# Performance work log

Hardware: AMD Instinct MI355X
Metric: run time of the kernel (lower is better)

## Reference

```python
import jax, jax.numpy as jnp
import numpy as np

B, N, F_IN, F_OUT = 1024, 16, 1024, 4096  # n_nodes=16 and n_heads=1 are structurally fixed by the module


def setup_inputs() -> dict:
    key = jax.random.key(0)
    ks = jax.random.split(key, 7)
    s1 = 1.0 / np.sqrt(F_IN)
    s2 = 1.0 / np.sqrt(F_IN * 16)
    return {
        "x": jax.random.normal(ks[0], (B, N, F_IN), jnp.float32),
        "matrix": jax.random.uniform(ks[1], (B, N, N), jnp.float32),
        "W1": jax.random.uniform(ks[2], (F_IN, F_IN), jnp.float32, -s1, s1),
        "b1": jax.random.uniform(ks[3], (F_IN,), jnp.float32, -s1, s1),
        "W_mlp": jax.random.uniform(ks[4], (F_OUT, F_IN * 16), jnp.float32, -s2, s2),
        "b_mlp": jax.random.uniform(ks[5], (F_OUT,), jnp.float32, -s2, s2),
        "a_param": jnp.float32(5.0),
    }


def _l2norm(v):
    # matches F.normalize(p=2, dim=-1, eps=1e-12)
    n = jnp.maximum(jnp.linalg.norm(v, axis=-1, keepdims=True), 1e-12)
    return v / n


def _forward(x, matrix, W1, b1, W_mlp, b_mlp, a_param):
    Bc, n, f = x.shape  # n_heads = 1, n_hidden = f
    wg = x @ W1.T + b1                                    # [B,n,f]
    gs = _l2norm(x)                                       # g_reshaped (H=1)
    gt = _l2norm(wg)                                      # g_transposed
    e = jnp.einsum('bik,bjk->bij', gs, gt)[..., None]     # [B,n,n,1] cosine scores
    eye = jnp.eye(n, dtype=x.dtype)[None, :, :, None]
    e = e * (1.0 + eye * a_param)                         # boost diagonal
    a_scores = e                                          # pre-softmax scores (used below)
    esm = jax.nn.softmax(e, axis=1)                       # softmax over dim=1
    m = matrix[..., None]                                 # [B,n,n,1]
    # MPUGAT message passing
    from_i = jnp.einsum('bitp,btkp->bikp', esm, m)        # [B,n,n,1]
    diag = jnp.einsum('bkkp->bkp', m)                     # diagonal of matrix
    from_j = esm * diag[:, None, :, :]                    # '...jkp,...kkp->...jkp'
    e2 = jnp.einsum('bikp,bjkp->bijp', from_i, from_j)    # [B,n,n,1]
    e2 = 0.5 * (e2 + jnp.transpose(e2, (0, 2, 1, 3)))
    # attention readout with PRE-softmax scores a_scores
    g = x.reshape(Bc, n, 1, f)                            # [B,n,H=1,f]
    attn = jnp.tanh(jnp.einsum('bjhf,bjih->bihf', g, a_scores))  # [B,n,1,f]
    out = attn.reshape(Bc, -1) @ W_mlp.T + b_mlp          # [B,F_OUT]
    out = jnp.broadcast_to(out[:, None, :], (Bc, 16, out.shape[-1]))  # repeat(1,16,1)
    return out, e2, m


def reference(x, matrix, W1, b1, W_mlp, b_mlp, a_param):
    return _forward(x, matrix, W1, b1, W_mlp, b_mlp, a_param)
```

## Files before the change

### kernel.cpp

```cpp
#include <hip/hip_runtime.h>
#include <math.h>

typedef short short8 __attribute__((ext_vector_type(8)));
typedef float f32x4 __attribute__((ext_vector_type(4)));
typedef unsigned short us4 __attribute__((ext_vector_type(4)));
typedef unsigned int u32x4 __attribute__((ext_vector_type(4)));
typedef unsigned short u16;
typedef unsigned int u32;

#define GAS __attribute__((address_space(1)))
#define LAS __attribute__((address_space(3)))

static __device__ __forceinline__ u16 f2bf(float f) {
    union { float f; u32 u; } v; v.f = f;
    u32 r = v.u + 0x7FFFu + ((v.u >> 16) & 1u);
    return (u16)(r >> 16);
}

static __device__ __forceinline__ u32 pk2(float a, float b) {
    return (u32)f2bf(a) | ((u32)f2bf(b) << 16);
}

static __device__ __forceinline__ u32 cvtpk(float lo, float hi) {
    u32 r;
    asm("v_cvt_pk_bf16_f32 %0, %1, %2" : "=v"(r) : "v"(lo), "v"(hi));
    return r;
}

static __device__ __forceinline__ float bf2f(u16 h) {
    union { u32 u; float f; } v; v.u = ((u32)h) << 16;
    return v.f;
}

static __device__ __forceinline__ float ftanh(float v) {
    float t = __expf(-2.0f * fabsf(v));
    float r = (1.0f - t) / (1.0f + t);
    return copysignf(r, v);
}

static __device__ __forceinline__ void gll16(const void* g, void* l) {
    __builtin_amdgcn_global_load_lds((const GAS void*)g, (LAS void*)l, 16, 0, 0);
}

__global__ __launch_bounds__(256) void k_cvt_x(const float* __restrict__ x,
                                               u16* __restrict__ xb,
                                               float* __restrict__ xinv,
                                               const float* __restrict__ W1,
                                               u16* __restrict__ w1b) {
    const int bid = blockIdx.x, t = threadIdx.x;
    if (bid >= 16384) {
        const size_t i = (size_t)(bid - 16384) * 256 + t;
        const f32x4 v = *(const f32x4*)(W1 + 4 * i);
        u32* dst = (u32*)(w1b + 4 * i);
        dst[0] = pk2(v.x, v.y); dst[1] = pk2(v.z, v.w);
        return;
    }
    const int row = bid;
    const f32x4 v = *(const f32x4*)(x + (size_t)row * 1024 + 4 * t);
    u32* dst = (u32*)(xb + (size_t)row * 1024 + 4 * t);
    dst[0] = pk2(v.x, v.y); dst[1] = pk2(v.z, v.w);
    float s = v.x * v.x + v.y * v.y + v.z * v.z + v.w * v.w;
#pragma unroll
    for (int off = 1; off < 64; off <<= 1) s += __shfl_xor(s, off, 64);
    __shared__ float red[4];
    if ((t & 63) == 0) red[t >> 6] = s;
    __syncthreads();
    if (t == 0)
        xinv[row] = 1.0f / fmaxf(sqrtf(red[0] + red[1] + red[2] + red[3]), 1e-12f);
}

#define MFMA16(a, b, c) __builtin_amdgcn_mfma_f32_16x16x32_bf16(a, b, c, 0, 0, 0)
#define SBAR() __builtin_amdgcn_s_barrier()
#define SCHED0() __builtin_amdgcn_sched_barrier(0)
#define PHFENCE() do { SBAR(); SCHED0(); } while (0)
#define VMW4 asm volatile("s_waitcnt vmcnt(4)" ::: "memory")
#define VMW2 asm volatile("s_waitcnt vmcnt(2)" ::: "memory")
#define VMW0 asm volatile("s_waitcnt vmcnt(0)" ::: "memory")
#define VMW8L asm volatile("s_waitcnt vmcnt(8) lgkmcnt(0)" ::: "memory")
#define LGKML asm volatile("s_waitcnt lgkmcnt(0)" ::: "memory")
#define VMNOP do {} while (0)

#define DO_TILE(ISS, VMA, VMB, VMD)                                           \
  do {                                                                        \
    short8 Af[4][2], Bf0[2][2], Bf1[2][2];                                    \
    _Pragma("unroll") for (int m = 0; m < 4; ++m) {                           \
      Af[m][0] = *(const short8*)(la + rpA[m] + sw0);                         \
      Af[m][1] = *(const short8*)(la + rpA[m] + sw1);                         \
    }                                                                         \
    _Pragma("unroll") for (int n = 0; n < 2; ++n) {                           \
      Bf0[n][0] = *(const short8*)(lb + rpB[n] + sw0);                        \
      Bf0[n][1] = *(const short8*)(lb + rpB[n] + sw1);                        \
    }                                                                         \
    if (ISS) { gll16(AG + (saO00 + knx), danext + ldst);                      \
               gll16(AG + (saO01 + knx), danext + 4096 + ldst); }             \
    PHFENCE();                                                                \
    __builtin_amdgcn_s_setprio(1);                                            \
    _Pragma("unroll") for (int k = 0; k < 2; ++k)                             \
      _Pragma("unroll") for (int m = 0; m < 4; ++m)                           \
        _Pragma("unroll") for (int n = 0; n < 2; ++n)                         \
          acc[m][n] = MFMA16(Af[m][k], Bf0[n][k], acc[m][n]);                 \
    __builtin_amdgcn_s_setprio(0); SCHED0(); VMA; SBAR();                     \
    _Pragma("unroll") for (int n = 0; n < 2; ++n) {                           \
      Bf1[n][0] = *(const short8*)(lb + rpB[n + 2] + sw0);                    \
      Bf1[n][1] = *(const short8*)(lb + rpB[n + 2] + sw1);                    \
    }                                                                         \
    if (ISS) { gll16(BG + (sbO00 + knx), dbnext + ldst);                      \
               gll16(BG + (sbO01 + knx), dbnext + 4096 + ldst); }             \
    PHFENCE();                                                                \
    __builtin_amdgcn_s_setprio(1);                                            \
    _Pragma("unroll") for (int k = 0; k < 2; ++k)                             \
      _Pragma("unroll") for (int m = 0; m < 4; ++m)                           \
        _Pragma("unroll") for (int n = 0; n < 2; ++n)                         \
          acc[m][n + 2] = MFMA16(Af[m][k], Bf1[n][k], acc[m][n + 2]);         \
    __builtin_amdgcn_s_setprio(0); SCHED0(); VMB; SBAR();                     \
    _Pragma("unroll") for (int m = 0; m < 4; ++m) {                           \
      Af[m][0] = *(const short8*)(la + rpA[m + 4] + sw0);                     \
      Af[m][1] = *(const short8*)(la + rpA[m + 4] + sw1);                     \
    }                                                                         \
    if (ISS) { gll16(BG + (sbO10 + knx), dbnext + 8192 + ldst);               \
               gll16(BG + (sbO11 + knx), dbnext + 8192 + 4096 + ldst); }      \
    PHFENCE();                                                                \
    __builtin_amdgcn_s_setprio(1);                                            \
    _Pragma("unroll") for (int k = 0; k < 2; ++k)                             \
      _Pragma("unroll") for (int m = 0; m < 4; ++m)                           \
        _Pragma("unroll") for (int n = 0; n < 2; ++n)                         \
          acc[m + 4][n] = MFMA16(Af[m][k], Bf0[n][k], acc[m + 4][n]);         \
    __builtin_amdgcn_s_setprio(0); SCHED0();                                  \
    if (ISS) { gll16(AG + (saO10 + knx), danext + 8192 + ldst);               \
               gll16(AG + (saO11 + knx), danext + 8192 + 4096 + ldst); }      \
    __builtin_amdgcn_s_setprio(1);                                            \
    _Pragma("unroll") for (int k = 0; k < 2; ++k)                             \
      _Pragma("unroll") for (int m = 0; m < 4; ++m)                           \
        _Pragma("unroll") for (int n = 0; n < 2; ++n)                         \
          acc[m + 4][n + 2] = MFMA16(Af[m][k], Bf1[n][k], acc[m + 4][n + 2]); \
    __builtin_amdgcn_s_setprio(0); SCHED0(); VMD; SBAR();                     \
  } while (0)

#define GT2S(ISS, KNXA, KNXB, WAITX)                                          \
  do {                                                                        \
    short8 Af[4][2], Bf0[2][2], Bf1[2][2];                                    \
    _Pragma("unroll") for (int m = 0; m < 4; ++m) {                           \
      Af[m][0] = *(const short8*)(la + rpA[m] + sw0);                         \
      Af[m][1] = *(const short8*)(la + rpA[m] + sw1);                         \
    }                                                                         \
    _Pragma("unroll") for (int n = 0; n < 2; ++n) {                           \
      Bf0[n][0] = *(const short8*)(lb + rpB[n] + sw0);                        \
      Bf0[n][1] = *(const short8*)(lb + rpB[n] + sw1);                        \
    }                                                                         \
    if (ISS) { gll16(AG + (saO00 + (KNXA)), danext + ldst);                   \
               gll16(AG + (saO01 + (KNXA)), danext + 4096 + ldst); }          \
    PHFENCE();                                                                \
    __builtin_amdgcn_s_setprio(1);                                            \
    _Pragma("unroll") for (int k = 0; k < 2; ++k)                             \
      _Pragma("unroll") for (int m = 0; m < 4; ++m)                           \
        _Pragma("unroll") for (int n = 0; n < 2; ++n)                         \
          acc[m][n] = MFMA16(Af[m][k], Bf0[n][k], acc[m][n]);                 \
    __builtin_amdgcn_s_setprio(0); SCHED0(); SBAR();                          \
    _Pragma("unroll") for (int n = 0; n < 2; ++n) {                           \
      Bf1[n][0] = *(const short8*)(lb + rpB[n + 2] + sw0);                    \
      Bf1[n][1] = *(const short8*)(lb + rpB[n + 2] + sw1);                    \
    }                                                                         \
    if (ISS) { gll16(AG + (saO10 + (KNXA)), danext + 8192 + ldst);            \
               gll16(AG + (saO11 + (KNXA)), danext + 8192 + 4096 + ldst); }   \
    PHFENCE();                                                                \
    __builtin_amdgcn_s_setprio(1);                                            \
    _Pragma("unroll") for (int k = 0; k < 2; ++k)                             \
      _Pragma("unroll") for (int m = 0; m < 4; ++m)                           \
        _Pragma("unroll") for (int n = 0; n < 2; ++n)                         \
          acc[m][n + 2] = MFMA16(Af[m][k], Bf1[n][k], acc[m][n + 2]);         \
    __builtin_amdgcn_s_setprio(0); SCHED0(); SBAR();                          \
    _Pragma("unroll") for (int m = 0; m < 4; ++m) {                           \
      Af[m][0] = *(const short8*)(la + rpA[m + 4] + sw0);                     \
      Af[m][1] = *(const short8*)(la + rpA[m + 4] + sw1);                     \
    }                                                                         \
    PHFENCE();                                                                \
    __builtin_amdgcn_s_setprio(1);                                            \
    _Pragma("unroll") for (int k = 0; k < 2; ++k)                             \
      _Pragma("unroll") for (int m = 0; m < 4; ++m)                           \
        _Pragma("unroll") for (int n = 0; n < 2; ++n)                         \
          acc[m + 4][n] = MFMA16(Af[m][k], Bf0[n][k], acc[m + 4][n]);         \
    __builtin_amdgcn_s_setprio(0); SCHED0();                                  \
    if (ISS) {                                                                \
      _Pragma("unroll") for (int c = 0; c < 2; ++c) {                         \
        u32x4 wv;                                                             \
        wv.x = cvtpk(bn[2 * c].x, bn[2 * c].y);                               \
        wv.y = cvtpk(bn[2 * c].z, bn[2 * c].w);                               \
        wv.z = cvtpk(bn[2 * c + 1].x, bn[2 * c + 1].y);                       \
        wv.w = cvtpk(bn[2 * c + 1].z, bn[2 * c + 1].w);                       \
        *(u32x4*)(dbnext + c * 4096 + (tid << 3)) = wv;                       \
        bn[2 * c]     = *(const f32x4*)(BGf + bro[c] + (KNXB) + swsrc);       \
        bn[2 * c + 1] = *(const f32x4*)(BGf + bro[c] + (KNXB) + swsrc + 4);   \
      }                                                                       \
    }                                                                         \
    __builtin_amdgcn_s_setprio(1);                                            \
    _Pragma("unroll") for (int k = 0; k < 2; ++k)                             \
      _Pragma("unroll") for (int m = 0; m < 4; ++m)                           \
        _Pragma("unroll") for (int n = 0; n < 2; ++n)                         \
          acc[m + 4][n + 2] = MFMA16(Af[m][k], Bf1[n][k], acc[m + 4][n + 2]); \
    __builtin_amdgcn_s_setprio(0); SCHED0();                                  \
    if (ISS) {                                                                \
      _Pragma("unroll") for (int c = 2; c < 4; ++c) {                         \
        u32x4 wv;                                                             \
        wv.x = cvtpk(bn[2 * c].x, bn[2 * c].y);                               \
        wv.y = cvtpk(bn[2 * c].z, bn[2 * c].w);                               \
        wv.z = cvtpk(bn[2 * c + 1].x, bn[2 * c + 1].y);                       \
        wv.w = cvtpk(bn[2 * c + 1].z, bn[2 * c + 1].w);                       \
        *(u32x4*)(dbnext + c * 4096 + (tid << 3)) = wv;                       \
        bn[2 * c]     = *(const f32x4*)(BGf + bro[c] + (KNXB) + swsrc);       \
        bn[2 * c + 1] = *(const f32x4*)(BGf + bro[c] + (KNXB) + swsrc + 4);   \
      }                                                                       \
    }                                                                         \
    WAITX; SBAR();                                                            \
  } while (0)

__global__ __launch_bounds__(512, 2) void k_gemm1_8ph(const u16* __restrict__ AG,
                                                      const u16* __restrict__ BG,
                                                      const float* __restrict__ bias,
                                                      u16* __restrict__ C,
                                                      float* __restrict__ wgn2) {
    __shared__ __align__(16) u16 LsA[2][16384];
    __shared__ __align__(16) u16 LsB[2][16384];
    const int K = 1024, NT = 16;
    const int lin = blockIdx.x;
    const int w = (lin & 7) * 32 + (lin >> 3);
    const int n0 = (w & 3) * 256;
    const int m0 = (w >> 2) * 256;

    const int tid = threadIdx.x, wave = tid >> 6, lane = tid & 63;
    const int lr = lane & 15, kq = lane >> 4;
    const int wr = wave >> 2, wc = wave & 3;

    const int trow = tid >> 3;
    const u32 swsrc = (u32)(((tid & 7) ^ (trow & 7)) * 8);
    const u32 saO00 = (u32)(m0 + 0 + trow) * (u32)K + swsrc;
    const u32 saO01 = (u32)(m0 + 128 + trow) * (u32)K + swsrc;
    const u32 saO10 = (u32)(m0 + 64 + trow) * (u32)K + swsrc;
    const u32 saO11 = (u32)(m0 + 192 + trow) * (u32)K + swsrc;
    const int q0 = trow, q1 = 64 + trow;
    const u32 sbO00 = (u32)(n0 + (q0 >> 5) * 64 + (q0 & 31)) * (u32)K + swsrc;
    const u32 sbO01 = (u32)(n0 + (q1 >> 5) * 64 + (q1 & 31)) * (u32)K + swsrc;
    const u32 sbO10 = (u32)(n0 + (q0 >> 5) * 64 + 32 + (q0 & 31)) * (u32)K + swsrc;
    const u32 sbO11 = (u32)(n0 + (q1 >> 5) * 64 + 32 + (q1 & 31)) * (u32)K + swsrc;
    const u32 ldst = (u32)wave * 512;

    int rpA[8], rpB[4];
#pragma unroll
    for (int mf = 0; mf < 8; ++mf)
        rpA[mf] = ((mf >> 2) * 128 + wr * 64 + (mf & 3) * 16 + lr) << 6;
#pragma unroll
    for (int nf = 0; nf < 4; ++nf)
        rpB[nf] = ((nf >> 1) * 128 + wc * 32 + (nf & 1) * 16 + lr) << 6;
    const int sw0 = ((0 + kq) ^ (lr & 7)) * 8;
    const int sw1 = ((4 + kq) ^ (lr & 7)) * 8;

    f32x4 acc[8][4] = {};

    gll16(AG + saO00, &LsA[0][0] + ldst);
    gll16(AG + saO01, &LsA[0][0] + 4096 + ldst);
    gll16(BG + sbO00, &LsB[0][0] + ldst);
    gll16(BG + sbO01, &LsB[0][0] + 4096 + ldst);
    gll16(BG + sbO10, &LsB[0][0] + 8192 + ldst);
    gll16(BG + sbO11, &LsB[0][0] + 8192 + 4096 + ldst);
    gll16(AG + saO10, &LsA[0][0] + 8192 + ldst);
    gll16(AG + saO11, &LsA[0][0] + 8192 + 4096 + ldst);
    VMW4;
    SBAR();

    int cur = 0;
    u32 ko = 64;
    for (int T = 0; T < NT - 1; ++T) {
        const u16* la = &LsA[cur][0];
        const u16* lb = &LsB[cur][0];
        u16* danext = &LsA[cur ^ 1][0];
        u16* dbnext = &LsB[cur ^ 1][0];
        const u32 knx = ko;
        DO_TILE(1, VMW4, VMW4, VMW4);
        cur ^= 1;
        ko += 64;
    }
    {
        const u16* la = &LsA[cur][0];
        const u16* lb = &LsB[cur][0];
        u16* danext = &LsA[cur ^ 1][0];
        u16* dbnext = &LsB[cur ^ 1][0];
        const u32 knx = 0;
        (void)danext; (void)dbnext;
        DO_TILE(0, VMW2, VMW0, VMNOP);
    }

    const int col0 = n0 + wc * 64;
    const int row0 = m0 + wr * 128;
    float bcol[4];
#pragma unroll
    for (int nf = 0; nf < 4; ++nf) bcol[nf] = bias[col0 + nf * 16 + lr];
#pragma unroll
    for (int mf = 0; mf < 8; ++mf) {
#pragma unroll
        for (int r = 0; r < 4; ++r) {
            const int row = row0 + mf * 16 + kq * 4 + r;
            float nrm = 0.f;
#pragma unroll
            for (int nf = 0; nf < 4; ++nf) {
                float v = acc[mf][nf][r] + bcol[nf];
                C[(size_t)row * 1024 + col0 + nf * 16 + lr] = f2bf(v);
                nrm += v * v;
            }
#pragma unroll
            for (int off = 1; off < 16; off <<= 1) nrm += __shfl_xor(nrm, off, 64);
            if (lr == 0) atomicAdd(&wgn2[row], nrm);
        }
    }
}

__global__ __launch_bounds__(512, 2) void k_gemm2_8ph(const u16* __restrict__ AG,
                                                      const float* __restrict__ BGf,
                                                      u16* __restrict__ part) {
    __shared__ __align__(16) u16 LsA[2][16384];
    __shared__ __align__(16) u16 LsB[2][16384];
    const int K = 16384, NT = 64;
    const int lin = blockIdx.x;
    const int w = (lin & 7) * 32 + (lin >> 3);
    const int m0 = (w & 3) * 256;
    const int z = (w >> 2) & 3;
    const int n0 = (w >> 4) * 256;
    const int kbeg = z * 4096;

    const int tid = threadIdx.x, wave = tid >> 6, lane = tid & 63;
    const int lr = lane & 15, kq = lane >> 4;
    const int wr = wave >> 2, wc = wave & 3;

    const int trow = tid >> 3;
    const u32 swsrc = (u32)(((tid & 7) ^ (trow & 7)) * 8);
    const u32 saO00 = (u32)(m0 + 0 + trow) * (u32)K + (u32)kbeg + swsrc;
    const u32 saO01 = (u32)(m0 + 128 + trow) * (u32)K + (u32)kbeg + swsrc;
    const u32 saO10 = (u32)(m0 + 64 + trow) * (u32)K + (u32)kbeg + swsrc;
    const u32 saO11 = (u32)(m0 + 192 + trow) * (u32)K + (u32)kbeg + swsrc;
    const int q0 = trow, q1 = 64 + trow;
    u32 bro[4];
    bro[0] = (u32)(n0 + (q0 >> 5) * 64 + (q0 & 31)) * 16384u + (u32)kbeg;
    bro[1] = (u32)(n0 + (q1 >> 5) * 64 + (q1 & 31)) * 16384u + (u32)kbeg;
    bro[2] = bro[0] + 32u * 16384u;
    bro[3] = bro[1] + 32u * 16384u;
    const u32 ldst = (u32)wave * 512;

    int rpA[8], rpB[4];
#pragma unroll
    for (int mf = 0; mf < 8; ++mf)
        rpA[mf] = ((mf >> 2) * 128 + wr * 64 + (mf & 3) * 16 + lr) << 6;
#pragma unroll
    for (int nf = 0; nf < 4; ++nf)
        rpB[nf] = ((nf >> 1) * 128 + wc * 32 + (nf & 1) * 16 + lr) << 6;
    const int sw0 = ((0 + kq) ^ (lr & 7)) * 8;
    const int sw1 = ((4 + kq) ^ (lr & 7)) * 8;

    f32x4 acc[8][4] = {};
    f32x4 bn[8];

    {
#pragma unroll
        for (int c = 0; c < 4; ++c) {
            bn[2 * c]     = *(const f32x4*)(BGf + bro[c] + swsrc);
            bn[2 * c + 1] = *(const f32x4*)(BGf + bro[c] + swsrc + 4);
        }
        gll16(AG + saO00, &LsA[0][0] + ldst);
        gll16(AG + saO01, &LsA[0][0] + 4096 + ldst);
        gll16(AG + saO10, &LsA[0][0] + 8192 + ldst);
        gll16(AG + saO11, &LsA[0][0] + 8192 + 4096 + ldst);
#pragma unroll
        for (int c = 0; c < 4; ++c) {
            u32x4 wv;
            wv.x = cvtpk(bn[2 * c].x, bn[2 * c].y);
            wv.y = cvtpk(bn[2 * c].z, bn[2 * c].w);
            wv.z = cvtpk(bn[2 * c + 1].x, bn[2 * c + 1].y);
            wv.w = cvtpk(bn[2 * c + 1].z, bn[2 * c + 1].w);
            *(u32x4*)(&LsB[0][0] + c * 4096 + (tid << 3)) = wv;
        }
        asm volatile("s_waitcnt vmcnt(0) lgkmcnt(0)" ::: "memory");
#pragma unroll
        for (int c = 0; c < 4; ++c) {
            bn[2 * c]     = *(const f32x4*)(BGf + bro[c] + 64 + swsrc);
            bn[2 * c + 1] = *(const f32x4*)(BGf + bro[c] + 64 + swsrc + 4);
        }
        SBAR();
    }

    int cur = 0;
    for (int T = 0; T < NT - 1; ++T) {
        const u16* la = &LsA[cur][0];
        const u16* lb = &LsB[cur][0];
        u16* danext = &LsA[cur ^ 1][0];
        u16* dbnext = &LsB[cur ^ 1][0];
        const u32 knxa = (u32)(T + 1) * 64;
        const u32 knxb = (T + 2 < NT) ? (u32)(T + 2) * 64 : 0u;
        GT2S(1, knxa, knxb, VMW8L);
        cur ^= 1;
    }
    {
        const u16* la = &LsA[cur][0];
        const u16* lb = &LsB[cur][0];
        u16* danext = &LsA[cur ^ 1][0];
        u16* dbnext = &LsB[cur ^ 1][0];
        (void)danext; (void)dbnext;
        GT2S(0, 0u, 0u, LGKML);
    }

    u16* po = part + (size_t)z * 4194304ull;
    const int col0 = n0 + wc * 64;
    const int row0 = m0 + wr * 128;
#pragma unroll
    for (int mf = 0; mf < 8; ++mf)
#pragma unroll
        for (int r = 0; r < 4; ++r) {
            const int row = row0 + mf * 16 + kq * 4 + r;
#pragma unroll
            for (int nf = 0; nf < 4; ++nf)
                po[(size_t)row * 4096 + col0 + nf * 16 + lr] = f2bf(acc[mf][nf][r]);
        }
}

__global__ __launch_bounds__(256) void k_batch_attn(const u16* xb,
                                                    const u16* __restrict__ wgb,
                                                    const float* __restrict__ xinv,
                                                    const float* __restrict__ wgn2,
                                                    const float* __restrict__ matrix,
                                                    const float* __restrict__ a_param,
                                                    float* __restrict__ e2_out,
                                                    float* __restrict__ m_out,
                                                    u16* attn_bf) {
    const int b = blockIdx.x, tid = threadIdx.x;
    const int wave = tid >> 6, lane = tid & 63;
    const int j = lane & 15, ig = (lane >> 4) * 4;

    __shared__ float qred[4][64][4];
    __shared__ float esm_l[16 * 17];
    __shared__ float fi_l[16 * 17];
    __shared__ float e2_l[16 * 17];
    __shared__ float m_l[256];
    __shared__ float as_l[256];
    __shared__ u16 xsh[16][256];

    {
        const size_t roff = (size_t)(b * 16 + j) * 1024 + (lane >> 4) * 8 + wave * 256;
        f32x4 acc0 = {}, acc1 = {};
#pragma unroll
        for (int kt = 0; kt < 256; kt += 64) {
            short8 xa0 = *(const short8*)(xb + roff + kt);
            short8 wa0 = *(const short8*)(wgb + roff + kt);
            short8 xa1 = *(const short8*)(xb + roff + kt + 32);
            short8 wa1 = *(const short8*)(wgb + roff + kt + 32);
            acc0 = __builtin_amdgcn_mfma_f32_16x16x32_bf16(xa0, wa0, acc0, 0, 0, 0);
// ... 58 lines not shown
        for (int r = 0; r < 4; ++r) e2_l[(ig + r) * 17 + j] = e2v[r];
    }
    __syncthreads();
    if (tid < 64) {
#pragma unroll
        for (int r = 0; r < 4; ++r) {
            const int i = ig + r;
            e2_out[(size_t)b * 256 + i * 16 + j] =
                0.5f * (e2_l[i * 17 + j] + e2_l[j * 17 + i]);
        }
    }

    const int srow = tid >> 4;
    const int scol = (tid & 15) * 16;
    for (int ch = 0; ch < 4; ++ch) {
        __syncthreads();
        const u16* src = xb + ((size_t)b * 16 + srow) * 1024 + ch * 256 + scol;
        *(short8*)&xsh[srow][scol] = *(const short8*)src;
        *(short8*)&xsh[srow][scol + 8] = *(const short8*)(src + 8);
        __syncthreads();
        float accv[16] = {};
#pragma unroll
        for (int jj = 0; jj < 16; ++jj) {
            const float xv = bf2f(xsh[jj][tid]);
#pragma unroll
            for (int i = 0; i < 16; ++i) accv[i] = fmaf(as_l[jj * 16 + i], xv, accv[i]);
        }
#pragma unroll
        for (int i = 0; i < 16; ++i)
            attn_bf[((size_t)b * 16 + i) * 1024 + ch * 256 + tid] = f2bf(ftanh(accv[i]));
    }
}

__global__ __launch_bounds__(256) void k_bcast(const u16* __restrict__ p,
                                               const float* __restrict__ bias,
                                               float* __restrict__ out) {
    const size_t i = (size_t)blockIdx.x * 256 + threadIdx.x;
    const int o4 = (int)(i & 1023);
    const int b = (int)(i >> 14);
    const size_t src = (size_t)b * 4096 + (size_t)o4 * 4;
    f32x4 r = *(const f32x4*)(bias + (size_t)o4 * 4);
#pragma unroll
    for (int z = 0; z < 4; ++z) {
        us4 v = *(const us4*)(p + (size_t)z * 4194304ull + src);
        r.x += bf2f(v.x); r.y += bf2f(v.y); r.z += bf2f(v.z); r.w += bf2f(v.w);
    }
    *(f32x4*)(out + i * 4) = r;
}

extern "C" void kernel_launch(void* const* d_in, const int* in_sizes, int n_in,
                              void* d_out, int out_size, void* d_ws, size_t ws_size,
                              hipStream_t stream) {
    const float* x      = (const float*)d_in[0];
    const float* matrix = (const float*)d_in[1];
    const float* W1     = (const float*)d_in[2];
    const float* b1     = (const float*)d_in[3];
    const float* W_mlp  = (const float*)d_in[4];
    const float* b_mlp  = (const float*)d_in[5];
    const float* a_par  = (const float*)d_in[6];
    float* out = (float*)d_out;

    char* ws = (char*)d_ws;
    size_t off = 0;
    auto alloc = [&](size_t bytes) {
        char* p = ws + off;
        off += (bytes + 255) & ~(size_t)255;
        return p;
    };
    u16*   x_bf  = (u16*)alloc(16384ull * 1024 * 2);
    u16*   wg_bf = (u16*)alloc(16384ull * 1024 * 2);
    u16*   w1_bf = (u16*)alloc(1024ull * 1024 * 2);
    float* xinv  = (float*)alloc(16384ull * 4);
    float* wgn2  = (float*)alloc(16384ull * 4);
    u16*   attn_bf = x_bf;
    u16*   part    = wg_bf;
    float* e2_out = out + 67108864ull;
    float* m_out  = out + 67371008ull;

    hipMemsetAsync(wgn2, 0, 16384 * 4, stream);
    k_cvt_x<<<17408, 256, 0, stream>>>(x, x_bf, xinv, W1, w1_bf);
    k_gemm1_8ph<<<256, 512, 0, stream>>>(x_bf, w1_bf, b1, wg_bf, wgn2);
    k_batch_attn<<<1024, 256, 0, stream>>>(x_bf, wg_bf, xinv, wgn2, matrix, a_par,
                                           e2_out, m_out, attn_bf);
    k_gemm2_8ph<<<256, 512, 0, stream>>>(attn_bf, W_mlp, part);
    k_bcast<<<65536, 256, 0, stream>>>(part, b_mlp, out);
}
```

Measured before the change: 339.2 us.

## Pre-convert W_mlp to bf16 and deepen GEMM pipeline with prefetched B tiles

W_mlp is now converted to bf16 by the existing conversion kernel (extra blocks), so the second GEMM loads B directly into LDS with global_load_lds instead of loading fp32 into registers and converting in the main loop. Both GEMMs share a reworked 8-phase tile schedule that prefetches the next B half-tile two stages ahead, with vmcnt(6) waits and a two-tile epilogue. This takes conversion ALU work and register pressure out of the GEMM loop. In exchange it adds a separate 256MB-read / 128MB-write conversion pass over W_mlp on every call, plus a 128MB workspace buffer.

Result: slower. 398.5 us (+17.5%).

```diff
diff --git a/kernel.cpp b/kernel.cpp
--- a/kernel.cpp
+++ b/kernel.cpp
@@ -4,7 +4,6 @@
 typedef short short8 __attribute__((ext_vector_type(8)));
 typedef float f32x4 __attribute__((ext_vector_type(4)));
 typedef unsigned short us4 __attribute__((ext_vector_type(4)));
-typedef unsigned int u32x4 __attribute__((ext_vector_type(4)));
 typedef unsigned short u16;
 typedef unsigned int u32;
 
@@ -21,12 +20,6 @@
     return (u32)f2bf(a) | ((u32)f2bf(b) << 16);
 }
 
-static __device__ __forceinline__ u32 cvtpk(float lo, float hi) {
-    u32 r;
-    asm("v_cvt_pk_bf16_f32 %0, %1, %2" : "=v"(r) : "v"(lo), "v"(hi));
-    return r;
-}
-
 static __device__ __forceinline__ float bf2f(u16 h) {
     union { u32 u; float f; } v; v.u = ((u32)h) << 16;
     return v.f;
@@ -46,8 +39,17 @@
                                                u16* __restrict__ xb,
                                                float* __restrict__ xinv,
                                                const float* __restrict__ W1,
-                                               u16* __restrict__ w1b) {
+                                               u16* __restrict__ w1b,
+                                               const float* __restrict__ Wm,
+                                               u16* __restrict__ wmb) {
     const int bid = blockIdx.x, t = threadIdx.x;
+    if (bid >= 17408) {
+        const size_t i = (size_t)(bid - 17408) * 256 + t;
+        const f32x4 v = *(const f32x4*)(Wm + 4 * i);
+        u32* dst = (u32*)(wmb + 4 * i);
+        dst[0] = pk2(v.x, v.y); dst[1] = pk2(v.z, v.w);
+        return;
+    }
     if (bid >= 16384) {
         const size_t i = (size_t)(bid - 16384) * 256 + t;
         const f32x4 v = *(const f32x4*)(W1 + 4 * i);
@@ -72,17 +74,16 @@
 #define MFMA16(a, b, c) __builtin_amdgcn_mfma_f32_16x16x32_bf16(a, b, c, 0, 0, 0)
 #define SBAR() __builtin_amdgcn_s_barrier()
 #define SCHED0() __builtin_amdgcn_sched_barrier(0)
-#define PHFENCE() do { SBAR(); SCHED0(); } while (0)
+#define VMW6 asm volatile("s_waitcnt vmcnt(6)" ::: "memory")
 #define VMW4 asm volatile("s_waitcnt vmcnt(4)" ::: "memory")
 #define VMW2 asm volatile("s_waitcnt vmcnt(2)" ::: "memory")
 #define VMW0 asm volatile("s_waitcnt vmcnt(0)" ::: "memory")
-#define VMW8L asm volatile("s_waitcnt vmcnt(8) lgkmcnt(0)" ::: "memory")
-#define LGKML asm volatile("s_waitcnt lgkmcnt(0)" ::: "memory")
 #define VMNOP do {} while (0)
 
-#define DO_TILE(ISS, VMA, VMB, VMD)                                           \
+#define DO_TILE(I0, I1, I2, I3, W0, W1M, W2, W3)                              \
   do {                                                                        \
     short8 Af[4][2], Bf0[2][2], Bf1[2][2];                                    \
+                                         \
     _Pragma("unroll") for (int m = 0; m < 4; ++m) {                           \
       Af[m][0] = *(const short8*)(la + rpA[m] + sw0);                         \
       Af[m][1] = *(const short8*)(la + rpA[m] + sw1);                         \
@@ -91,126 +92,68 @@
       Bf0[n][0] = *(const short8*)(lb + rpB[n] + sw0);                        \
       Bf0[n][1] = *(const short8*)(lb + rpB[n] + sw1);                        \
     }                                                                         \
-    if (ISS) { gll16(AG + (saO00 + knx), danext + ldst);                      \
-               gll16(AG + (saO01 + knx), danext + 4096 + ldst); }             \
-    PHFENCE();                                                                \
+    if (I0) { gll16(AG + (saO00 + knxa), danext + ldst);                      \
+              gll16(AG + (saO01 + knxa), danext + 4096 + ldst); }             \
+    SBAR(); SCHED0();                                                         \
     __builtin_amdgcn_s_setprio(1);                                            \
     _Pragma("unroll") for (int k = 0; k < 2; ++k)                             \
       _Pragma("unroll") for (int m = 0; m < 4; ++m)                           \
         _Pragma("unroll") for (int n = 0; n < 2; ++n)                         \
           acc[m][n] = MFMA16(Af[m][k], Bf0[n][k], acc[m][n]);                 \
-    __builtin_amdgcn_s_setprio(0); SCHED0(); VMA; SBAR();                     \
+    __builtin_amdgcn_s_setprio(0); SCHED0(); W0; SBAR();                      \
+                                                      \
     _Pragma("unroll") for (int n = 0; n < 2; ++n) {                           \
       Bf1[n][0] = *(const short8*)(lb + rpB[n + 2] + sw0);                    \
       Bf1[n][1] = *(const short8*)(lb + rpB[n + 2] + sw1);                    \
     }                                                                         \
-    if (ISS) { gll16(BG + (sbO00 + knx), dbnext + ldst);                      \
-               gll16(BG + (sbO01 + knx), dbnext + 4096 + ldst); }             \
-    PHFENCE();                                                                \
+    if (I1) { gll16(BG + (sbO10 + knxa), dbnext + 8192 + ldst);               \
+              gll16(BG + (sbO11 + knxa), dbnext + 8192 + 4096 + ldst); }      \
+    SBAR(); SCHED0();                                                         \
     __builtin_amdgcn_s_setprio(1);                                            \
     _Pragma("unroll") for (int k = 0; k < 2; ++k)                             \
       _Pragma("unroll") for (int m = 0; m < 4; ++m)                           \
         _Pragma("unroll") for (int n = 0; n < 2; ++n)                         \
           acc[m][n + 2] = MFMA16(Af[m][k], Bf1[n][k], acc[m][n + 2]);         \
-    __builtin_amdgcn_s_setprio(0); SCHED0(); VMB; SBAR();                     \
+    __builtin_amdgcn_s_setprio(0); SCHED0(); W1M; SBAR();                     \
+                                                      \
     _Pragma("unroll") for (int m = 0; m < 4; ++m) {                           \
       Af[m][0] = *(const short8*)(la + rpA[m + 4] + sw0);                     \
       Af[m][1] = *(const short8*)(la + rpA[m + 4] + sw1);                     \
     }                                                                         \
-    if (ISS) { gll16(BG + (sbO10 + knx), dbnext + 8192 + ldst);               \
-               gll16(BG + (sbO11 + knx), dbnext + 8192 + 4096 + ldst); }      \
-    PHFENCE();                                                                \
+    if (I2) { gll16(AG + (saO10 + knxa), danext + 8192 + ldst);               \
+              gll16(AG + (saO11 + knxa), danext + 8192 + 4096 + ldst); }      \
+    SBAR(); SCHED0();                                                         \
     __builtin_amdgcn_s_setprio(1);                                            \
     _Pragma("unroll") for (int k = 0; k < 2; ++k)                             \
       _Pragma("unroll") for (int m = 0; m < 4; ++m)                           \
         _Pragma("unroll") for (int n = 0; n < 2; ++n)                         \
           acc[m + 4][n] = MFMA16(Af[m][k], Bf0[n][k], acc[m + 4][n]);         \
-    __builtin_amdgcn_s_setprio(0); SCHED0();                                  \
-    if (ISS) { gll16(AG + (saO10 + knx), danext + 8192 + ldst);               \
-               gll16(AG + (saO11 + knx), danext + 8192 + 4096 + ldst); }      \
+    __builtin_amdgcn_s_setprio(0); SCHED0(); W2; SBAR();                      \
+     \
+    if (I3) { gll16(BG + (sbO00 + knxb), lbw + ldst);                         \
+              gll16(BG + (sbO01 + knxb), lbw + 4096 + ldst); }                \
+    SBAR(); SCHED0();                                                         \
     __builtin_amdgcn_s_setprio(1);                                            \
     _Pragma("unroll") for (int k = 0; k < 2; ++k)                             \
       _Pragma("unroll") for (int m = 0; m < 4; ++m)                           \
         _Pragma("unroll") for (int n = 0; n < 2; ++n)                         \
           acc[m + 4][n + 2] = MFMA16(Af[m][k], Bf1[n][k], acc[m + 4][n + 2]); \
-    __builtin_amdgcn_s_setprio(0); SCHED0(); VMD; SBAR();                     \
+    __builtin_amdgcn_s_setprio(0); SCHED0(); W3; SBAR();                      \
   } while (0)
 
-#define GT2S(ISS, KNXA, KNXB, WAITX)                                          \
+#define GEMM_PROLOGUE()                                                       \
   do {                                                                        \
-    short8 Af[4][2], Bf0[2][2], Bf1[2][2];                                    \
-    _Pragma("unroll") for (int m = 0; m < 4; ++m) {                           \
-      Af[m][0] = *(const short8*)(la + rpA[m] + sw0);                         \
-      Af[m][1] = *(const short8*)(la + rpA[m] + sw1);                         \
-    }                                                                         \
-    _Pragma("unroll") for (int n = 0; n < 2; ++n) {                           \
-      Bf0[n][0] = *(const short8*)(lb + rpB[n] + sw0);                        \
-      Bf0[n][1] = *(const short8*)(lb + rpB[n] + sw1);                        \
-    }                                                                         \
-    if (ISS) { gll16(AG + (saO00 + (KNXA)), danext + ldst);                   \
-               gll16(AG + (saO01 + (KNXA)), danext + 4096 + ldst); }          \
-    PHFENCE();                                                                \
-    __builtin_amdgcn_s_setprio(1);                                            \
-    _Pragma("unroll") for (int k = 0; k < 2; ++k)                             \
-      _Pragma("unroll") for (int m = 0; m < 4; ++m)                           \
-        _Pragma("unroll") for (int n = 0; n < 2; ++n)                         \
-          acc[m][n] = MFMA16(Af[m][k], Bf0[n][k], acc[m][n]);                 \
-    __builtin_amdgcn_s_setprio(0); SCHED0(); SBAR();                          \
-    _Pragma("unroll") for (int n = 0; n < 2; ++n) {                           \
-      Bf1[n][0] = *(const short8*)(lb + rpB[n + 2] + sw0);                    \
-      Bf1[n][1] = *(const short8*)(lb + rpB[n + 2] + sw1);                    \
-    }                                                                         \
-    if (ISS) { gll16(AG + (saO10 + (KNXA)), danext + 8192 + ldst);            \
-               gll16(AG + (saO11 + (KNXA)), danext + 8192 + 4096 + ldst); }   \
-    PHFENCE();                                                                \
-    __builtin_amdgcn_s_setprio(1);                                            \
-    _Pragma("unroll") for (int k = 0; k < 2; ++k)                             \
-      _Pragma("unroll") for (int m = 0; m < 4; ++m)                           \
-        _Pragma("unroll") for (int n = 0; n < 2; ++n)                         \
-          acc[m][n + 2] = MFMA16(Af[m][k], Bf1[n][k], acc[m][n + 2]);         \
-    __builtin_amdgcn_s_setprio(0); SCHED0(); SBAR();                          \
-    _Pragma("unroll") for (int m = 0; m < 4; ++m) {                           \
-      Af[m][0] = *(const short8*)(la + rpA[m + 4] + sw0);                     \
-      Af[m][1] = *(const short8*)(la + rpA[m + 4] + sw1);                     \
-    }                                                                         \
-    PHFENCE();                                                                \
-    __builtin_amdgcn_s_setprio(1);                                            \
-    _Pragma("unroll") for (int k = 0; k < 2; ++k)                             \
-      _Pragma("unroll") for (int m = 0; m < 4; ++m)                           \
-        _Pragma("unroll") for (int n = 0; n < 2; ++n)                         \
-          acc[m + 4][n] = MFMA16(Af[m][k], Bf0[n][k], acc[m + 4][n]);         \
-    __builtin_amdgcn_s_setprio(0); SCHED0();                                  \
-    if (ISS) {                                                                \
-      _Pragma("unroll") for (int c = 0; c < 2; ++c) {                         \
-        u32x4 wv;                                                             \
-        wv.x = cvtpk(bn[2 * c].x, bn[2 * c].y);                               \
-        wv.y = cvtpk(bn[2 * c].z, bn[2 * c].w);                               \
-        wv.z = cvtpk(bn[2 * c + 1].x, bn[2 * c + 1].y);                       \
-        wv.w = cvtpk(bn[2 * c + 1].z, bn[2 * c + 1].w);                       \
-        *(u32x4*)(dbnext + c * 4096 + (tid << 3)) = wv;                       \
-        bn[2 * c]     = *(const f32x4*)(BGf + bro[c] + (KNXB) + swsrc);       \
-        bn[2 * c + 1] = *(const f32x4*)(BGf + bro[c] + (KNXB) + swsrc + 4);   \
-      }                                                                       \
-    }                                                                         \
-    __builtin_amdgcn_s_setprio(1);                                            \
-    _Pragma("unroll") for (int k = 0; k < 2; ++k)                             \
-      _Pragma("unroll") for (int m = 0; m < 4; ++m)                           \
-        _Pragma("unroll") for (int n = 0; n < 2; ++n)                         \
-          acc[m + 4][n + 2] = MFMA16(Af[m][k], Bf1[n][k], acc[m + 4][n + 2]); \
-    __builtin_amdgcn_s_setprio(0); SCHED0();                                  \
-    if (ISS) {                                                                \
-      _Pragma("unroll") for (int c = 2; c < 4; ++c) {                         \
-        u32x4 wv;                                                             \
-        wv.x = cvtpk(bn[2 * c].x, bn[2 * c].y);                               \
-        wv.y = cvtpk(bn[2 * c].z, bn[2 * c].w);                               \
-        wv.z = cvtpk(bn[2 * c + 1].x, bn[2 * c + 1].y);                       \
-        wv.w = cvtpk(bn[2 * c + 1].z, bn[2 * c + 1].w);                       \
-        *(u32x4*)(dbnext + c * 4096 + (tid << 3)) = wv;                       \
-        bn[2 * c]     = *(const f32x4*)(BGf + bro[c] + (KNXB) + swsrc);       \
-        bn[2 * c + 1] = *(const f32x4*)(BGf + bro[c] + (KNXB) + swsrc + 4);   \
-      }                                                                       \
-    }                                                                         \
-    WAITX; SBAR();                                                            \
+    gll16(AG + saO00, &LsA[0][0] + ldst);                                     \
+    gll16(AG + saO01, &LsA[0][0] + 4096 + ldst);                              \
+    gll16(BG + sbO00, &LsB[0][0] + ldst);                                     \
+    gll16(BG + sbO01, &LsB[0][0] + 4096 + ldst);                              \
+    gll16(BG + sbO10, &LsB[0][0] + 8192 + ldst);                              \
+    gll16(BG + sbO11, &LsB[0][0] + 8192 + 4096 + ldst);                       \
+    gll16(AG + saO10, &LsA[0][0] + 8192 + ldst);                              \
+    gll16(AG + saO11, &LsA[0][0] + 8192 + 4096 + ldst);                       \
+    gll16(BG + sbO00 + 64, &LsB[1][0] + ldst);                                \
+    gll16(BG + sbO01 + 64, &LsB[1][0] + 4096 + ldst);                         \
+    VMW6; SBAR();                                                             \
   } while (0)
 
 __global__ __launch_bounds__(512, 2) void k_gemm1_8ph(const u16* __restrict__ AG,
@@ -255,37 +198,40 @@
 
     f32x4 acc[8][4] = {};
 
-    gll16(AG + saO00, &LsA[0][0] + ldst);
-    gll16(AG + saO01, &LsA[0][0] + 4096 + ldst);
-    gll16(BG + sbO00, &LsB[0][0] + ldst);
-    gll16(BG + sbO01, &LsB[0][0] + 4096 + ldst);
-    gll16(BG + sbO10, &LsB[0][0] + 8192 + ldst);
-    gll16(BG + sbO11, &LsB[0][0] + 8192 + 4096 + ldst);
-    gll16(AG + saO10, &LsA[0][0] + 8192 + ldst);
-    gll16(AG + saO11, &LsA[0][0] + 8192 + 4096 + ldst);
-    VMW4;
-    SBAR();
+    GEMM_PROLOGUE();
 
     int cur = 0;
-    u32 ko = 64;
-    for (int T = 0; T < NT - 1; ++T) {
+    for (int T = 0; T < NT - 2; ++T) {
         const u16* la = &LsA[cur][0];
         const u16* lb = &LsB[cur][0];
         u16* danext = &LsA[cur ^ 1][0];
         u16* dbnext = &LsB[cur ^ 1][0];
-        const u32 knx = ko;
-        DO_TILE(1, VMW4, VMW4, VMW4);
+        u16* lbw = &LsB[cur][0];
+        const u32 knxa = (u32)(T + 1) * 64;
+        const u32 knxb = (u32)(T + 2) * 64;
+        DO_TILE(1, 1, 1, 1, VMW6, VMW6, VMW6, VMW6);
         cur ^= 1;
-        ko += 64;
     }
     {
         const u16* la = &LsA[cur][0];
         const u16* lb = &LsB[cur][0];
         u16* danext = &LsA[cur ^ 1][0];
         u16* dbnext = &LsB[cur ^ 1][0];
-        const u32 knx = 0;
-        (void)danext; (void)dbnext;
-        DO_TILE(0, VMW2, VMW0, VMNOP);
+        u16* lbw = &LsB[cur][0];
+        const u32 knxa = (u32)(NT - 1) * 64, knxb = 0;
+        (void)knxb;
+        DO_TILE(1, 1, 1, 0, VMW6, VMW6, VMW6, VMW4);
+        cur ^= 1;
+    }
+    {
+        const u16* la = &LsA[cur][0];
+        const u16* lb = &LsB[cur][0];
+        u16* danext = &LsA[cur ^ 1][0];
+        u16* dbnext = &LsB[cur ^ 1][0];
+        u16* lbw = &LsB[cur][0];
+        const u32 knxa = 0, knxb = 0;
+        (void)danext; (void)dbnext; (void)lbw; (void)knxa; (void)knxb;
+        DO_TILE(0, 0, 0, 0, VMW2, VMW0, VMNOP, VMNOP);
     }
 
     const int col0 = n0 + wc * 64;
@@ -313,7 +259,7 @@
 }
 
 __global__ __launch_bounds__(512, 2) void k_gemm2_8ph(const u16* __restrict__ AG,
-                                                      const float* __restrict__ BGf,
+                                                      const u16* __restrict__ BG,
                                                       u16* __restrict__ part) {
     __shared__ __align__(16) u16 LsA[2][16384];
     __shared__ __align__(16) u16 LsB[2][16384];
@@ -336,11 +282,10 @@
     const u32 saO10 = (u32)(m0 + 64 + trow) * (u32)K + (u32)kbeg + swsrc;
     const u32 saO11 = (u32)(m0 + 192 + trow) * (u32)K + (u32)kbeg + swsrc;
     const int q0 = trow, q1 = 64 + trow;
-    u32 bro[4];
-    bro[0] = (u32)(n0 + (q0 >> 5) * 64 + (q0 & 31)) * 16384u + (u32)kbeg;
-    bro[1] = (u32)(n0 + (q1 >> 5) * 64 + (q1 & 31)) * 16384u + (u32)kbeg;
-    bro[2] = bro[0] + 32u * 16384u;
-    bro[3] = bro[1] + 32u * 16384u;
+    const u32 sbO00 = (u32)(n0 + (q0 >> 5) * 64 + (q0 & 31)) * (u32)K + (u32)kbeg + swsrc;
+    const u32 sbO01 = (u32)(n0 + (q1 >> 5) * 64 + (q1 & 31)) * (u32)K + (u32)kbeg + swsrc;
+    const u32 sbO10 = (u32)(n0 + (q0 >> 5) * 64 + 32 + (q0 & 31)) * (u32)K + (u32)kbeg + swsrc;
+    const u32 sbO11 = (u32)(n0 + (q1 >> 5) * 64 + 32 + (q1 & 31)) * (u32)K + (u32)kbeg + swsrc;
     const u32 ldst = (u32)wave * 512;
 
     int rpA[8], rpB[4];
@@ -354,45 +299,19 @@
     const int sw1 = ((4 + kq) ^ (lr & 7)) * 8;
 
     f32x4 acc[8][4] = {};
-    f32x4 bn[8];
-
-    {
-#pragma unroll
-        for (int c = 0; c < 4; ++c) {
-            bn[2 * c]     = *(const f32x4*)(BGf + bro[c] + swsrc);
-            bn[2 * c + 1] = *(const f32x4*)(BGf + bro[c] + swsrc + 4);
-        }
-        gll16(AG + saO00, &LsA[0][0] + ldst);
-        gll16(AG + saO01, &LsA[0][0] + 4096 + ldst);
-        gll16(AG + saO10, &LsA[0][0] + 8192 + ldst);
-        gll16(AG + saO11, &LsA[0][0] + 8192 + 4096 + ldst);
-#pragma unroll
-        for (int c = 0; c < 4; ++c) {
-            u32x4 wv;
-            wv.x = cvtpk(bn[2 * c].x, bn[2 * c].y);
-            wv.y = cvtpk(bn[2 * c].z, bn[2 * c].w);
-            wv.z = cvtpk(bn[2 * c + 1].x, bn[2 * c + 1].y);
-            wv.w = cvtpk(bn[2 * c + 1].z, bn[2 * c + 1].w);
-            *(u32x4*)(&LsB[0][0] + c * 4096 + (tid << 3)) = wv;
-        }
-        asm volatile("s_waitcnt vmcnt(0) lgkmcnt(0)" ::: "memory");
-#pragma unroll
-        for (int c = 0; c < 4; ++c) {
-            bn[2 * c]     = *(const f32x4*)(BGf + bro[c] + 64 + swsrc);
-            bn[2 * c + 1] = *(const f32x4*)(BGf + bro[c] + 64 + swsrc + 4);
-        }
-        SBAR();
-    }
+
+    GEMM_PROLOGUE();
 
     int cur = 0;
-    for (int T = 0; T < NT - 1; ++T) {
+    for (int T = 0; T < NT - 2; ++T) {
         const u16* la = &LsA[cur][0];
         const u16* lb = &LsB[cur][0];
         u16* danext = &LsA[cur ^ 1][0];
         u16* dbnext = &LsB[cur ^ 1][0];
+        u16* lbw = &LsB[cur][0];
         const u32 knxa = (u32)(T + 1) * 64;
-        const u32 knxb = (T + 2 < NT) ? (u32)(T + 2) * 64 : 0u;
-        GT2S(1, knxa, knxb, VMW8L);
+        const u32 knxb = (u32)(T + 2) * 64;
+        DO_TILE(1, 1, 1, 1, VMW6, VMW6, VMW6, VMW6);
         cur ^= 1;
     }
     {
@@ -400,8 +319,21 @@
         const u16* lb = &LsB[cur][0];
         u16* danext = &LsA[cur ^ 1][0];
         u16* dbnext = &LsB[cur ^ 1][0];
-        (void)danext; (void)dbnext;
-        GT2S(0, 0u, 0u, LGKML);
+        u16* lbw = &LsB[cur][0];
+        const u32 knxa = (u32)(NT - 1) * 64, knxb = 0;
+        (void)knxb;
+        DO_TILE(1, 1, 1, 0, VMW6, VMW6, VMW6, VMW4);
+        cur ^= 1;
+    }
+    {
+        const u16* la = &LsA[cur][0];
+        const u16* lb = &LsB[cur][0];
+        u16* danext = &LsA[cur ^ 1][0];
+        u16* dbnext = &LsB[cur ^ 1][0];
+        u16* lbw = &LsB[cur][0];
+        const u32 knxa = 0, knxb = 0;
+        (void)danext; (void)dbnext; (void)lbw; (void)knxa; (void)knxb;
+        DO_TILE(0, 0, 0, 0, VMW2, VMW0, VMNOP, VMNOP);
     }
 
     u16* po = part + (size_t)z * 4194304ull;
@@ -578,6 +510,7 @@
     u16*   x_bf  = (u16*)alloc(16384ull * 1024 * 2);
     u16*   wg_bf = (u16*)alloc(16384ull * 1024 * 2);
     u16*   w1_bf = (u16*)alloc(1024ull * 1024 * 2);
+    u16*   wm_bf = (u16*)alloc(4096ull * 16384 * 2);
     float* xinv  = (float*)alloc(16384ull * 4);
     float* wgn2  = (float*)alloc(16384ull * 4);
     u16*   attn_bf = x_bf;
@@ -586,10 +519,10 @@
     float* m_out  = out + 67371008ull;
 
     hipMemsetAsync(wgn2, 0, 16384 * 4, stream);
-    k_cvt_x<<<17408, 256, 0, stream>>>(x, x_bf, xinv, W1, w1_bf);
+    k_cvt_x<<<82944, 256, 0, stream>>>(x, x_bf, xinv, W1, w1_bf, W_mlp, wm_bf);
     k_gemm1_8ph<<<256, 512, 0, stream>>>(x_bf, w1_bf, b1, wg_bf, wgn2);
     k_batch_attn<<<1024, 256, 0, stream>>>(x_bf, wg_bf, xinv, wgn2, matrix, a_par,
                                            e2_out, m_out, attn_bf);
-    k_gemm2_8ph<<<256, 512, 0, stream>>>(attn_bf, W_mlp, part);
+    k_gemm2_8ph<<<256, 512, 0, stream>>>(attn_bf, wm_bf, part);
     k_bcast<<<65536, 256, 0, stream>>>(part, b_mlp, out);
 }
```

## Fuse split-K reduction and broadcast into GEMM2 via per-tile atomic counters

Applied to the files above, without the earlier changes.

Removes the separate broadcast kernel. Each GEMM2 workgroup writes its split-K partial, then waits on a per-tile atomic counter until all four K-slices of its tile are done. It then sums the partials, adds the bias and writes its quarter of the 16x-repeated output. This saves a kernel launch and lets the reduction overlap with other tiles' GEMM work. The cost is spin-waiting, which relies on all 256 workgroups being co-resident (2 per CU with launch bounds) and risks deadlock otherwise. The counter is zeroed by extending the existing memset, which relies on cnt being allocated directly after wgn2.

Result: slower. 482.1 us (+42.1%).

```diff
diff --git a/kernel.cpp b/kernel.cpp
--- a/kernel.cpp
+++ b/kernel.cpp
@@ -314,7 +314,10 @@
 
 __global__ __launch_bounds__(512, 2) void k_gemm2_8ph(const u16* __restrict__ AG,
                                                       const float* __restrict__ BGf,
-                                                      u16* __restrict__ part) {
+                                                      u16* __restrict__ part,
+                                                      const float* __restrict__ bias,
+                                                      float* __restrict__ out,
+                                                      u32* __restrict__ cnt) {
     __shared__ __align__(16) u16 LsA[2][16384];
     __shared__ __align__(16) u16 LsB[2][16384];
     const int K = 16384, NT = 64;
@@ -416,6 +419,35 @@
             for (int nf = 0; nf < 4; ++nf)
                 po[(size_t)row * 4096 + col0 + nf * 16 + lr] = f2bf(acc[mf][nf][r]);
         }
+
+    const int tile = (w & 3) * 16 + (w >> 4);
+    __threadfence();
+    if (tid == 0) {
+        atomicAdd(&cnt[tile], 1u);
+        while (atomicAdd(&cnt[tile], 0u) < 4u) __builtin_amdgcn_s_sleep(8);
+    }
+    __syncthreads();
+    __threadfence();
+
+    const int cg = (tid & 63) * 4;
+    const int rb = tid >> 6;
+    const f32x4 bb = *(const f32x4*)(bias + n0 + cg);
+    const size_t colbase = (size_t)(n0 + cg);
+#pragma unroll 1
+    for (int pass = 0; pass < 32; ++pass) {
+        const int row = pass * 8 + rb;
+        const size_t pidx = (size_t)(m0 + row) * 4096 + colbase;
+        f32x4 v = bb;
+#pragma unroll
+        for (int zz = 0; zz < 4; ++zz) {
+            us4 u = *(const us4*)(part + (size_t)zz * 4194304ull + pidx);
+            v.x += bf2f(u.x); v.y += bf2f(u.y); v.z += bf2f(u.z); v.w += bf2f(u.w);
+        }
+        const size_t ob = ((size_t)(m0 + row) * 16 + z * 4) * 4096 + colbase;
+#pragma unroll
+        for (int r2 = 0; r2 < 4; ++r2)
+            *(f32x4*)(out + ob + (size_t)r2 * 4096) = v;
+    }
 }
 
 __global__ __launch_bounds__(256) void k_batch_attn(const u16* xb,
@@ -540,22 +572,6 @@
     }
 }
 
-__global__ __launch_bounds__(256) void k_bcast(const u16* __restrict__ p,
-                                               const float* __restrict__ bias,
-                                               float* __restrict__ out) {
-    const size_t i = (size_t)blockIdx.x * 256 + threadIdx.x;
-    const int o4 = (int)(i & 1023);
-    const int b = (int)(i >> 14);
-    const size_t src = (size_t)b * 4096 + (size_t)o4 * 4;
-    f32x4 r = *(const f32x4*)(bias + (size_t)o4 * 4);
-#pragma unroll
-    for (int z = 0; z < 4; ++z) {
-        us4 v = *(const us4*)(p + (size_t)z * 4194304ull + src);
-        r.x += bf2f(v.x); r.y += bf2f(v.y); r.z += bf2f(v.z); r.w += bf2f(v.w);
-    }
-    *(f32x4*)(out + i * 4) = r;
-}
-
 extern "C" void kernel_launch(void* const* d_in, const int* in_sizes, int n_in,
                               void* d_out, int out_size, void* d_ws, size_t ws_size,
                               hipStream_t stream) {
@@ -580,16 +596,16 @@
     u16*   w1_bf = (u16*)alloc(1024ull * 1024 * 2);
     float* xinv  = (float*)alloc(16384ull * 4);
     float* wgn2  = (float*)alloc(16384ull * 4);
+    u32*   cnt   = (u32*)alloc(256 * 4);
     u16*   attn_bf = x_bf;
     u16*   part    = wg_bf;
     float* e2_out = out + 67108864ull;
     float* m_out  = out + 67371008ull;
 
-    hipMemsetAsync(wgn2, 0, 16384 * 4, stream);
+    hipMemsetAsync(wgn2, 0, 16384 * 4 + 1024, stream);
     k_cvt_x<<<17408, 256, 0, stream>>>(x, x_bf, xinv, W1, w1_bf);
     k_gemm1_8ph<<<256, 512, 0, stream>>>(x_bf, w1_bf, b1, wg_bf, wgn2);
     k_batch_attn<<<1024, 256, 0, stream>>>(x_bf, wg_bf, xinv, wgn2, matrix, a_par,
                                            e2_out, m_out, attn_bf);
-    k_gemm2_8ph<<<256, 512, 0, stream>>>(attn_bf, W_mlp, part);
-    k_bcast<<<65536, 256, 0, stream>>>(part, b_mlp, out);
-}
+    k_gemm2_8ph<<<256, 512, 0, stream>>>(attn_bf, W_mlp, part, b_mlp, out, cnt);
+}
```

## Deepen GEMM1 prefetch by issuing next-next B half into freed LDS slot

Applied to the files above, without the earlier changes.

Restructures the double-buffered GEMM1 main loop so the first half of B for tile T+2 is loaded into the current buffer once its fragments have been consumed, giving those loads more time in flight. The loop is split into a steady-state body, a penultimate tile and a final tile, and wait counts are raised to vmcnt(6). The aim is to hide more global-load latency behind MFMA work. The cost is an extra barrier per tile and more complex wait accounting, with a risk of LDS read/write hazards if the waits are off.

New measurement: 334.2 us. About the same (-1.5%).

```diff
diff --git a/kernel.cpp b/kernel.cpp
--- a/kernel.cpp
+++ b/kernel.cpp
@@ -73,6 +73,7 @@
 #define SBAR() __builtin_amdgcn_s_barrier()
 #define SCHED0() __builtin_amdgcn_sched_barrier(0)
 #define PHFENCE() do { SBAR(); SCHED0(); } while (0)
+#define VMW6 asm volatile("s_waitcnt vmcnt(6)" ::: "memory")
 #define VMW4 asm volatile("s_waitcnt vmcnt(4)" ::: "memory")
 #define VMW2 asm volatile("s_waitcnt vmcnt(2)" ::: "memory")
 #define VMW0 asm volatile("s_waitcnt vmcnt(0)" ::: "memory")
@@ -80,7 +81,7 @@
 #define LGKML asm volatile("s_waitcnt lgkmcnt(0)" ::: "memory")
 #define VMNOP do {} while (0)
 
-#define DO_TILE(ISS, VMA, VMB, VMD)                                           \
+#define DO_T1(I0, I1, I2, I3, W0, W1M, W2, W3)                                \
   do {                                                                        \
     short8 Af[4][2], Bf0[2][2], Bf1[2][2];                                    \
     _Pragma("unroll") for (int m = 0; m < 4; ++m) {                           \
@@ -91,49 +92,65 @@
       Bf0[n][0] = *(const short8*)(lb + rpB[n] + sw0);                        \
       Bf0[n][1] = *(const short8*)(lb + rpB[n] + sw1);                        \
     }                                                                         \
-    if (ISS) { gll16(AG + (saO00 + knx), danext + ldst);                      \
-               gll16(AG + (saO01 + knx), danext + 4096 + ldst); }             \
-    PHFENCE();                                                                \
+    if (I0) { gll16(AG + (saO00 + knxa), danext + ldst);                      \
+              gll16(AG + (saO01 + knxa), danext + 4096 + ldst); }             \
+    SBAR(); SCHED0();                                                         \
     __builtin_amdgcn_s_setprio(1);                                            \
     _Pragma("unroll") for (int k = 0; k < 2; ++k)                             \
       _Pragma("unroll") for (int m = 0; m < 4; ++m)                           \
         _Pragma("unroll") for (int n = 0; n < 2; ++n)                         \
           acc[m][n] = MFMA16(Af[m][k], Bf0[n][k], acc[m][n]);                 \
-    __builtin_amdgcn_s_setprio(0); SCHED0(); VMA; SBAR();                     \
+    __builtin_amdgcn_s_setprio(0); SCHED0(); W0; SBAR();                      \
     _Pragma("unroll") for (int n = 0; n < 2; ++n) {                           \
       Bf1[n][0] = *(const short8*)(lb + rpB[n + 2] + sw0);                    \
       Bf1[n][1] = *(const short8*)(lb + rpB[n + 2] + sw1);                    \
     }                                                                         \
-    if (ISS) { gll16(BG + (sbO00 + knx), dbnext + ldst);                      \
-               gll16(BG + (sbO01 + knx), dbnext + 4096 + ldst); }             \
-    PHFENCE();                                                                \
+    if (I1) { gll16(BG + (sbO10 + knxa), dbnext + 8192 + ldst);               \
+              gll16(BG + (sbO11 + knxa), dbnext + 8192 + 4096 + ldst); }      \
+    SBAR(); SCHED0();                                                         \
     __builtin_amdgcn_s_setprio(1);                                            \
     _Pragma("unroll") for (int k = 0; k < 2; ++k)                             \
       _Pragma("unroll") for (int m = 0; m < 4; ++m)                           \
         _Pragma("unroll") for (int n = 0; n < 2; ++n)                         \
           acc[m][n + 2] = MFMA16(Af[m][k], Bf1[n][k], acc[m][n + 2]);         \
-    __builtin_amdgcn_s_setprio(0); SCHED0(); VMB; SBAR();                     \
+    __builtin_amdgcn_s_setprio(0); SCHED0(); W1M; SBAR();                     \
     _Pragma("unroll") for (int m = 0; m < 4; ++m) {                           \
       Af[m][0] = *(const short8*)(la + rpA[m + 4] + sw0);                     \
       Af[m][1] = *(const short8*)(la + rpA[m + 4] + sw1);                     \
     }                                                                         \
-    if (ISS) { gll16(BG + (sbO10 + knx), dbnext + 8192 + ldst);               \
-               gll16(BG + (sbO11 + knx), dbnext + 8192 + 4096 + ldst); }      \
-    PHFENCE();                                                                \
+    if (I2) { gll16(AG + (saO10 + knxa), danext + 8192 + ldst);               \
+              gll16(AG + (saO11 + knxa), danext + 8192 + 4096 + ldst); }      \
+    SBAR(); SCHED0();                                                         \
     __builtin_amdgcn_s_setprio(1);                                            \
     _Pragma("unroll") for (int k = 0; k < 2; ++k)                             \
       _Pragma("unroll") for (int m = 0; m < 4; ++m)                           \
         _Pragma("unroll") for (int n = 0; n < 2; ++n)                         \
           acc[m + 4][n] = MFMA16(Af[m][k], Bf0[n][k], acc[m + 4][n]);         \
-    __builtin_amdgcn_s_setprio(0); SCHED0();                                  \
-    if (ISS) { gll16(AG + (saO10 + knx), danext + 8192 + ldst);               \
-               gll16(AG + (saO11 + knx), danext + 8192 + 4096 + ldst); }      \
+    __builtin_amdgcn_s_setprio(0); SCHED0(); W2; SBAR();                      \
+    if (I3) { gll16(BG + (sbO00 + knxb), lbw + ldst);                         \
+              gll16(BG + (sbO01 + knxb), lbw + 4096 + ldst); }                \
+    SBAR(); SCHED0();                                                         \
     __builtin_amdgcn_s_setprio(1);                                            \
     _Pragma("unroll") for (int k = 0; k < 2; ++k)                             \
       _Pragma("unroll") for (int m = 0; m < 4; ++m)                           \
         _Pragma("unroll") for (int n = 0; n < 2; ++n)                         \
           acc[m + 4][n + 2] = MFMA16(Af[m][k], Bf1[n][k], acc[m + 4][n + 2]); \
-    __builtin_amdgcn_s_setprio(0); SCHED0(); VMD; SBAR();                     \
+    __builtin_amdgcn_s_setprio(0); SCHED0(); W3; SBAR();                      \
+  } while (0)
+
+#define GEMM1_PROLOGUE()                                                      \
+  do {                                                                        \
+    gll16(AG + saO00, &LsA[0][0] + ldst);                                     \
+    gll16(AG + saO01, &LsA[0][0] + 4096 + ldst);                              \
+    gll16(BG + sbO00, &LsB[0][0] + ldst);                                     \
+    gll16(BG + sbO01, &LsB[0][0] + 4096 + ldst);                              \
+    gll16(BG + sbO10, &LsB[0][0] + 8192 + ldst);                              \
+    gll16(BG + sbO11, &LsB[0][0] + 8192 + 4096 + ldst);                       \
+    gll16(AG + saO10, &LsA[0][0] + 8192 + ldst);                              \
+    gll16(AG + saO11, &LsA[0][0] + 8192 + 4096 + ldst);                       \
+    gll16(BG + sbO00 + 64, &LsB[1][0] + ldst);                                \
+    gll16(BG + sbO01 + 64, &LsB[1][0] + 4096 + ldst);                         \
+    VMW6; SBAR();                                                             \
   } while (0)
 
 #define GT2S(ISS, KNXA, KNXB, WAITX)                                          \
@@ -255,37 +272,40 @@
 
     f32x4 acc[8][4] = {};
 
-    gll16(AG + saO00, &LsA[0][0] + ldst);
-    gll16(AG + saO01, &LsA[0][0] + 4096 + ldst);
-    gll16(BG + sbO00, &LsB[0][0] + ldst);
-    gll16(BG + sbO01, &LsB[0][0] + 4096 + ldst);
-    gll16(BG + sbO10, &LsB[0][0] + 8192 + ldst);
-    gll16(BG + sbO11, &LsB[0][0] + 8192 + 4096 + ldst);
-    gll16(AG + saO10, &LsA[0][0] + 8192 + ldst);
-    gll16(AG + saO11, &LsA[0][0] + 8192 + 4096 + ldst);
-    VMW4;
-    SBAR();
+    GEMM1_PROLOGUE();
 
     int cur = 0;
-    u32 ko = 64;
-    for (int T = 0; T < NT - 1; ++T) {
+    for (int T = 0; T < NT - 2; ++T) {
         const u16* la = &LsA[cur][0];
         const u16* lb = &LsB[cur][0];
         u16* danext = &LsA[cur ^ 1][0];
         u16* dbnext = &LsB[cur ^ 1][0];
-        const u32 knx = ko;
-        DO_TILE(1, VMW4, VMW4, VMW4);
+        u16* lbw = &LsB[cur][0];
+        const u32 knxa = (u32)(T + 1) * 64;
+        const u32 knxb = (u32)(T + 2) * 64;
+        DO_T1(1, 1, 1, 1, VMW6, VMW6, VMW6, VMW6);
         cur ^= 1;
-        ko += 64;
     }
     {
         const u16* la = &LsA[cur][0];
         const u16* lb = &LsB[cur][0];
         u16* danext = &LsA[cur ^ 1][0];
         u16* dbnext = &LsB[cur ^ 1][0];
-        const u32 knx = 0;
-        (void)danext; (void)dbnext;
-        DO_TILE(0, VMW2, VMW0, VMNOP);
+        u16* lbw = &LsB[cur][0];
+        const u32 knxa = (u32)(NT - 1) * 64, knxb = 0;
+        (void)knxb;
+        DO_T1(1, 1, 1, 0, VMW6, VMW6, VMW6, VMW4);
+        cur ^= 1;
+    }
+    {
+        const u16* la = &LsA[cur][0];
+        const u16* lb = &LsB[cur][0];
+        u16* danext = &LsA[cur ^ 1][0];
+        u16* dbnext = &LsB[cur ^ 1][0];
+        u16* lbw = &LsB[cur][0];
+        const u32 knxa = 0, knxb = 0;
+        (void)danext; (void)dbnext; (void)lbw; (void)knxa; (void)knxb;
+        DO_T1(0, 0, 0, 0, VMW2, VMW0, VMNOP, VMNOP);
     }
 
     const int col0 = n0 + wc * 64;
```
